# Kernel optimization log

Measured on AMD Instinct MI355X. Metric: run time of the kernel, lower is better.

The kernel has to match this reference:

```python
import jax, jax.numpy as jnp
import numpy as np

N = 100001      # item_num + 1
D = 64          # hidden_units
NNZ = 3200000   # number of nonzeros in encoder_adj (avg degree ~32)


def setup_inputs() -> dict:
    key = jax.random.key(0)
    k1, k2, k3, k4 = jax.random.split(key, 4)
    row_idx = jax.random.randint(k1, (NNZ,), 0, N, dtype=jnp.int32)
    col_idx = jax.random.randint(k2, (NNZ,), 0, N, dtype=jnp.int32)
    adj_vals = jax.random.uniform(k3, (NNZ,), dtype=jnp.float32)
    emb_weight = jax.random.normal(k4, (N, D), dtype=jnp.float32)
    return {"row_idx": row_idx, "col_idx": col_idx, "adj_vals": adj_vals,
            "emb_weight": emb_weight}


def _spmm(row_idx, col_idx, vals, x):
    # COO SpMM: out[r] += vals[e] * x[col[e]]  -> [N, D]
    gathered = vals[:, None] * x[col_idx]          # [NNZ, D]
    return jax.ops.segment_sum(gathered, row_idx, num_segments=N)


def reference(row_idx, col_idx, adj_vals, emb_weight):
    e0 = emb_weight                                 # ego embeddings
    e1 = _spmm(row_idx, col_idx, adj_vals, e0)      # GCN layer 1
    e2 = _spmm(row_idx, col_idx, adj_vals, e1)      # GCN layer 2
    summed = e0 + e1 + e2                           # sum(embeds)
    return (summed, e0, e1, e2)
```

## Files before the change

### kernel.cpp

```cpp
#include <hip/hip_runtime.h>
#include <stdint.h>

#define DHID 64
#define G_BLOCKS 256
#define BMAX 2048
#define RPB 64

static inline size_t align256(size_t x) { return (x + 255) & ~(size_t)255; }


__global__ void zero_f32(float* __restrict__ p, size_t n) {
  size_t i = (size_t)blockIdx.x * blockDim.x + threadIdx.x;
  if (i < n) p[i] = 0.f;
}


__global__ void a1_hist_k(const int* __restrict__ row, int* __restrict__ histGB,
                          int nnz, int B, int chunk) {
  __shared__ int h[BMAX];
  for (int i = threadIdx.x; i < B; i += blockDim.x) h[i] = 0;
  __syncthreads();
  int g = blockIdx.x;
  int s = g * chunk, e = min(nnz, s + chunk);
  for (int j = s + threadIdx.x; j < e; j += blockDim.x)
    atomicAdd(&h[row[j] >> 6], 1);
  __syncthreads();
  for (int i = threadIdx.x; i < B; i += blockDim.x)
    histGB[i * G_BLOCKS + g] = h[i];
}

__global__ void scan_gb_k(const int* __restrict__ histGB, int* __restrict__ offGB,
                          int* __restrict__ btot, int B) {
  __shared__ int wsum[4];
  int b = blockIdx.x, t = threadIdx.x, lane = t & 63, w = t >> 6;
  int v = histGB[b * G_BLOCKS + t];
  int incl = v;
#pragma unroll
  for (int off = 1; off < 64; off <<= 1) {
    int u = __shfl_up(incl, off);
    if (lane >= off) incl += u;
  }
  if (lane == 63) wsum[w] = incl;
  __syncthreads();
  int woff = 0;
  for (int w2 = 0; w2 < w; ++w2) woff += wsum[w2];
  offGB[b * G_BLOCKS + t] = woff + incl - v;
  if (t == 0) btot[b] = wsum[0] + wsum[1] + wsum[2] + wsum[3];
}

__global__ void scan_b_k(const int* __restrict__ btot, int* __restrict__ base, int B) {
  __shared__ int wsum[4];
  int t = threadIdx.x, lane = t & 63, w = t >> 6;
  int v[8];
  int s = 0;
#pragma unroll
  for (int i = 0; i < 8; ++i) {
    int idx = t * 8 + i;
    v[i] = (idx < B) ? btot[idx] : 0;
    s += v[i];
  }
  int incl = s;
#pragma unroll
  for (int off = 1; off < 64; off <<= 1) {
    int u = __shfl_up(incl, off);
    if (lane >= off) incl += u;
  }
  if (lane == 63) wsum[w] = incl;
  __syncthreads();
  int run = incl - s;
  for (int w2 = 0; w2 < w; ++w2) run += wsum[w2];
#pragma unroll
  for (int i = 0; i < 8; ++i) {
    int idx = t * 8 + i;
    if (idx <= B) base[idx] = run;
    run += v[i];
  }
}

__global__ void a2_scatter_k(const int* __restrict__ row, const int* __restrict__ col,
                             const float* __restrict__ val, const int* __restrict__ base,
                             const int* __restrict__ offGB, int2* __restrict__ stage,
                             int nnz, int B, int chunk) {
  __shared__ int cur[BMAX];
  int g = blockIdx.x;
  for (int i = threadIdx.x; i < B; i += blockDim.x)
    cur[i] = base[i] + offGB[i * G_BLOCKS + g];
  __syncthreads();
  int s = g * chunk, e = min(nnz, s + chunk);
  for (int j = s + threadIdx.x; j < e; j += blockDim.x) {
    int r = row[j];
    int b = r >> 6;
    int pos = atomicAdd(&cur[b], 1);
    int2 p;
    p.x = ((r & 63) << 24) | col[j];
    p.y = __float_as_int(val[j]);
    stage[pos] = p;
  }
}


__global__ __launch_bounds__(256) void
bgroup_k(const int* __restrict__ base, const int2* __restrict__ stage,
         int2* __restrict__ edges, int* __restrict__ rowstart, int n, int nnz) {
  __shared__ int h[RPB];
  __shared__ int cur[RPB];
  int b = blockIdx.x, t = threadIdx.x;
  if (t < RPB) h[t] = 0;
  __syncthreads();
  int s = base[b], e = base[b + 1];
  for (int j = s + t; j < e; j += 256)
    atomicAdd(&h[((unsigned)stage[j].x) >> 24], 1);
  __syncthreads();
  if (t < RPB) {
    int v = h[t];
    int incl = v;
#pragma unroll
    for (int off = 1; off < 64; off <<= 1) {
      int u = __shfl_up(incl, off);
      if (t >= off) incl += u;
    }
    int excl = incl - v;
    cur[t] = s + excl;
    int r = (b << 6) + t;
    if (r < n) rowstart[r] = s + excl;
  }
  if (b == 0 && t == 0) rowstart[n] = nnz;
  __syncthreads();
  for (int j = s + t; j < e; j += 256) {
    int2 p = stage[j];
    int rlow = ((unsigned)p.x) >> 24;
    int pos = atomicAdd(&cur[rlow], 1);
    int2 q;
    q.x = p.x & 0xFFFFFF;
    q.y = p.y;
    edges[pos] = q;
  }
}


__global__ void spmm_k(const int* __restrict__ rowstart, const int2* __restrict__ edges,
                       const float* __restrict__ x, float* __restrict__ y, int n) {
  int wave = (blockIdx.x * blockDim.x + threadIdx.x) >> 6;
  int lane = threadIdx.x & 63;
  if (wave >= n) return;
  int start = __builtin_amdgcn_readfirstlane(rowstart[wave]);
  int end   = __builtin_amdgcn_readfirstlane(rowstart[wave + 1]);
  float acc = 0.f;
  int k = start;
  for (; k + 8 <= end; k += 8) {
    int2 e0 = edges[k + 0], e1 = edges[k + 1], e2 = edges[k + 2], e3 = edges[k + 3];
    int2 e4 = edges[k + 4], e5 = edges[k + 5], e6 = edges[k + 6], e7 = edges[k + 7];
    float x0 = x[((size_t)e0.x << 6) + lane];
    float x1 = x[((size_t)e1.x << 6) + lane];
    float x2 = x[((size_t)e2.x << 6) + lane];
    float x3 = x[((size_t)e3.x << 6) + lane];
    float x4 = x[((size_t)e4.x << 6) + lane];
    float x5 = x[((size_t)e5.x << 6) + lane];
    float x6 = x[((size_t)e6.x << 6) + lane];
    float x7 = x[((size_t)e7.x << 6) + lane];
    acc += __int_as_float(e0.y) * x0;
    acc += __int_as_float(e1.y) * x1;
    acc += __int_as_float(e2.y) * x2;
    acc += __int_as_float(e3.y) * x3;
    acc += __int_as_float(e4.y) * x4;
    acc += __int_as_float(e5.y) * x5;
    acc += __int_as_float(e6.y) * x6;
    acc += __int_as_float(e7.y) * x7;
  }
  for (; k < end; ++k) {
    int2 e = edges[k];
    acc += __int_as_float(e.y) * x[((size_t)e.x << 6) + lane];
  }
  y[((size_t)wave << 6) + lane] = acc;
}

__global__ void spmm_fused_k(const int* __restrict__ rowstart, const int2* __restrict__ edges,
                             const float* __restrict__ e0, const float* __restrict__ e1,
                             float* __restrict__ e2, float* __restrict__ summed,
                             float* __restrict__ e0out, int n) {
  int wave = (blockIdx.x * blockDim.x + threadIdx.x) >> 6;
  int lane = threadIdx.x & 63;
  if (wave >= n) return;
  int start = __builtin_amdgcn_readfirstlane(rowstart[wave]);
  int end   = __builtin_amdgcn_readfirstlane(rowstart[wave + 1]);
  float acc = 0.f;
  int k = start;
  for (; k + 8 <= end; k += 8) {
    int2 ea = edges[k + 0], eb = edges[k + 1], ec = edges[k + 2], ed = edges[k + 3];
    int2 ee = edges[k + 4], ef = edges[k + 5], eg = edges[k + 6], eh = edges[k + 7];
    float x0 = e1[((size_t)ea.x << 6) + lane];
    float x1 = e1[((size_t)eb.x << 6) + lane];
    float x2 = e1[((size_t)ec.x << 6) + lane];
    float x3 = e1[((size_t)ed.x << 6) + lane];
    float x4 = e1[((size_t)ee.x << 6) + lane];
    float x5 = e1[((size_t)ef.x << 6) + lane];
    float x6 = e1[((size_t)eg.x << 6) + lane];
    float x7 = e1[((size_t)eh.x << 6) + lane];
    acc += __int_as_float(ea.y) * x0;
    acc += __int_as_float(eb.y) * x1;
    acc += __int_as_float(ec.y) * x2;
    acc += __int_as_float(ed.y) * x3;
    acc += __int_as_float(ee.y) * x4;
    acc += __int_as_float(ef.y) * x5;
    acc += __int_as_float(eg.y) * x6;
    acc += __int_as_float(eh.y) * x7;
  }
  for (; k < end; ++k) {
    int2 e = edges[k];
    acc += __int_as_float(e.y) * e1[((size_t)e.x << 6) + lane];
  }
  size_t o = ((size_t)wave << 6) + lane;
  float v0 = e0[o];
  float v1 = e1[o];
  e2[o] = acc;
  summed[o] = v0 + v1 + acc;
  e0out[o] = v0;
}


__global__ void spmm_atomic_k(const int* __restrict__ row, const int* __restrict__ col,
                              const float* __restrict__ val, const float* __restrict__ x,
                              float* __restrict__ y, int nnz) {
  int wave = (blockIdx.x * blockDim.x + threadIdx.x) >> 6;
  int lane = threadIdx.x & 63;
  if (wave >= nnz) return;
  int r = row[wave]; int c = col[wave]; float v = val[wave];
  atomicAdd(&y[(size_t)r * DHID + lane], v * x[(size_t)c * DHID + lane]);
}

__global__ void sum_k(const float4* __restrict__ e0, const float4* __restrict__ e1,
                      const float4* __restrict__ e2, float4* __restrict__ summed,
                      float4* __restrict__ e0out, int n4) {
  int i = blockIdx.x * blockDim.x + threadIdx.x;
  if (i < n4) {
    float4 a = e0[i], b = e1[i], c = e2[i];
    float4 s;
    s.x = a.x + b.x + c.x;
    s.y = a.y + b.y + c.y;
    s.z = a.z + b.z + c.z;
    s.w = a.w + b.w + c.w;
    summed[i] = s;
    e0out[i] = a;
  }
}

extern "C" void kernel_launch(void* const* d_in, const int* in_sizes, int n_in,
                              void* d_out, int out_size, void* d_ws, size_t ws_size,
                              hipStream_t stream) {
  const int*   row = (const int*)d_in[0];
  const int*   col = (const int*)d_in[1];
  const float* val = (const float*)d_in[2];
  const float* emb = (const float*)d_in[3];
  int nnz = in_sizes[0];
  int n   = in_sizes[3] / DHID;
  size_t ND = (size_t)n * DHID;

  float* out    = (float*)d_out;
  float* summed = out;
  float* e0o    = out + ND;
  float* e1     = out + 2 * ND;
  float* e2     = out + 3 * ND;

  int B  = (n + RPB - 1) / RPB;
  int chunk = (nnz + G_BLOCKS - 1) / G_BLOCKS;

  size_t o0 = 0;
  size_t histGB_off   = o0; o0 += align256((size_t)BMAX * G_BLOCKS * 4);
  size_t offGB_off    = o0; o0 += align256((size_t)BMAX * G_BLOCKS * 4);
  size_t btot_off     = o0; o0 += align256((size_t)BMAX * 4);
  size_t base_off     = o0; o0 += align256((size_t)(BMAX + 1) * 4);
  size_t rowstart_off = o0; o0 += align256((size_t)(n + 1) * 4);
  size_t stage_off    = o0; o0 += align256((size_t)nnz * 8);
  size_t edges_off    = o0; o0 += align256((size_t)nnz * 8);
  size_t need_sorted = o0;

  bool use_sorted = (ws_size >= need_sorted) && (B <= BMAX) && (n < (1 << 24));

  int rb = (int)((ND + 255) / 256);
  int n4 = (int)(ND / 4);
  int sb = (n4 + 255) / 256;
  int wb = (int)(((size_t)nnz * 64 + 255) / 256);

  if (use_sorted) {
    uint8_t* w = (uint8_t*)d_ws;
    int*  histGB   = (int*)(w + histGB_off);
    int*  offGB    = (int*)(w + offGB_off);
    int*  btot     = (int*)(w + btot_off);
    int*  base     = (int*)(w + base_off);
    int*  rowstart = (int*)(w + rowstart_off);
    int2* stage    = (int2*)(w + stage_off);
    int2* edges    = (int2*)(w + edges_off);

    a1_hist_k<<<G_BLOCKS, 256, 0, stream>>>(row, histGB, nnz, B, chunk);
    scan_gb_k<<<B, 256, 0, stream>>>(histGB, offGB, btot, B);
    scan_b_k<<<1, 256, 0, stream>>>(btot, base, B);
    a2_scatter_k<<<G_BLOCKS, 256, 0, stream>>>(row, col, val, base, offGB, stage,
                                               nnz, B, chunk);
    bgroup_k<<<B, 256, 0, stream>>>(base, stage, edges, rowstart, n, nnz);

    spmm_k<<<rb, 256, 0, stream>>>(rowstart, edges, emb, e1, n);
    spmm_fused_k<<<rb, 256, 0, stream>>>(rowstart, edges, emb, e1, e2, summed, e0o, n);
  } else {
    zero_f32<<<(int)((ND + 255) / 256), 256, 0, stream>>>(e1, ND);
    spmm_atomic_k<<<wb, 256, 0, stream>>>(row, col, val, emb, e1, nnz);
    zero_f32<<<(int)((ND + 255) / 256), 256, 0, stream>>>(e2, ND);
    spmm_atomic_k<<<wb, 256, 0, stream>>>(row, col, val, e1, e2, nnz);
    sum_k<<<sb, 256, 0, stream>>>((const float4*)emb, (const float4*)e1,
                                  (const float4*)e2, (float4*)summed,
                                  (float4*)e0o, n4);
  }
}
```

Measured before the change: 492.2 us.

## Widen CSR-build partitioning: more scatter blocks, 128-row buckets, unrolled atomic loops

Changes the two-pass COO-to-CSR bucket sort to use 1024 partition blocks and 128-row buckets (782 buckets) instead of 256 blocks and 64-row buckets. The scan kernel now handles four partition counts per thread, and the bucket-group kernel runs a two-wave scan over 128 rows. The histogram, scatter and group loops are unrolled by four so more independent loads are in flight before the LDS atomics. This targets the preprocessing cost of too few scatter blocks for the GPU. In exchange, the per-block histogram and offset tables are larger, and each bucket-group block now sorts twice as many edges.

```diff
diff --git a/kernel.cpp b/kernel.cpp
--- a/kernel.cpp
+++ b/kernel.cpp
@@ -2,9 +2,9 @@
 #include <stdint.h>
 
 #define DHID 64
-#define G_BLOCKS 256
-#define BMAX 2048
-#define RPB 64
+#define G_BLOCKS 1024
+#define BMAX 1024
+#define RPB 128
 
 static inline size_t align256(size_t x) { return (x + 255) & ~(size_t)255; }
 
@@ -15,26 +15,42 @@
 }
 
 
-__global__ void a1_hist_k(const int* __restrict__ row, int* __restrict__ histGB,
-                          int nnz, int B, int chunk) {
+__global__ __launch_bounds__(256) void
+a1_hist_k(const int* __restrict__ row, int* __restrict__ histGB,
+          int nnz, int B, int chunk) {
   __shared__ int h[BMAX];
-  for (int i = threadIdx.x; i < B; i += blockDim.x) h[i] = 0;
+  for (int i = threadIdx.x; i < B; i += 256) h[i] = 0;
   __syncthreads();
   int g = blockIdx.x;
   int s = g * chunk, e = min(nnz, s + chunk);
-  for (int j = s + threadIdx.x; j < e; j += blockDim.x)
-    atomicAdd(&h[row[j] >> 6], 1);
-  __syncthreads();
-  for (int i = threadIdx.x; i < B; i += blockDim.x)
+  int j = s + threadIdx.x;
+  for (; j + 768 < e; j += 1024) {
+    int r0 = row[j], r1 = row[j + 256], r2 = row[j + 512], r3 = row[j + 768];
+    atomicAdd(&h[r0 >> 7], 1);
+    atomicAdd(&h[r1 >> 7], 1);
+    atomicAdd(&h[r2 >> 7], 1);
+    atomicAdd(&h[r3 >> 7], 1);
+  }
+  for (; j < e; j += 256)
+    atomicAdd(&h[row[j] >> 7], 1);
+  __syncthreads();
+  for (int i = threadIdx.x; i < B; i += 256)
     histGB[i * G_BLOCKS + g] = h[i];
 }
 
-__global__ void scan_gb_k(const int* __restrict__ histGB, int* __restrict__ offGB,
-                          int* __restrict__ btot, int B) {
+__global__ __launch_bounds__(256) void
+scan_gb_k(const int* __restrict__ histGB, int* __restrict__ offGB,
+          int* __restrict__ btot, int B) {
   __shared__ int wsum[4];
   int b = blockIdx.x, t = threadIdx.x, lane = t & 63, w = t >> 6;
-  int v = histGB[b * G_BLOCKS + t];
-  int incl = v;
+  int v[4];
+  int s4 = 0;
+#pragma unroll
+  for (int i = 0; i < 4; ++i) {
+    v[i] = histGB[b * G_BLOCKS + t * 4 + i];
+    s4 += v[i];
+  }
+  int incl = s4;
 #pragma unroll
   for (int off = 1; off < 64; off <<= 1) {
     int u = __shfl_up(incl, off);
@@ -42,9 +58,13 @@
   }
   if (lane == 63) wsum[w] = incl;
   __syncthreads();
-  int woff = 0;
-  for (int w2 = 0; w2 < w; ++w2) woff += wsum[w2];
-  offGB[b * G_BLOCKS + t] = woff + incl - v;
+  int run = incl - s4;
+  for (int w2 = 0; w2 < w; ++w2) run += wsum[w2];
+#pragma unroll
+  for (int i = 0; i < 4; ++i) {
+    offGB[b * G_BLOCKS + t * 4 + i] = run;
+    run += v[i];
+  }
   if (t == 0) btot[b] = wsum[0] + wsum[1] + wsum[2] + wsum[3];
 }
 
@@ -77,22 +97,40 @@
   }
 }
 
-__global__ void a2_scatter_k(const int* __restrict__ row, const int* __restrict__ col,
-                             const float* __restrict__ val, const int* __restrict__ base,
-                             const int* __restrict__ offGB, int2* __restrict__ stage,
-                             int nnz, int B, int chunk) {
+__global__ __launch_bounds__(256) void
+a2_scatter_k(const int* __restrict__ row, const int* __restrict__ col,
+             const float* __restrict__ val, const int* __restrict__ base,
+             const int* __restrict__ offGB, int2* __restrict__ stage,
+             int nnz, int B, int chunk) {
   __shared__ int cur[BMAX];
   int g = blockIdx.x;
-  for (int i = threadIdx.x; i < B; i += blockDim.x)
+  for (int i = threadIdx.x; i < B; i += 256)
     cur[i] = base[i] + offGB[i * G_BLOCKS + g];
   __syncthreads();
   int s = g * chunk, e = min(nnz, s + chunk);
-  for (int j = s + threadIdx.x; j < e; j += blockDim.x) {
+  int j = s + threadIdx.x;
+  for (; j + 768 < e; j += 1024) {
+    int r0 = row[j], r1 = row[j + 256], r2 = row[j + 512], r3 = row[j + 768];
+    int c0 = col[j], c1 = col[j + 256], c2 = col[j + 512], c3 = col[j + 768];
+    float v0 = val[j], v1 = val[j + 256], v2 = val[j + 512], v3 = val[j + 768];
+    int p0 = atomicAdd(&cur[r0 >> 7], 1);
+    int p1 = atomicAdd(&cur[r1 >> 7], 1);
+    int p2 = atomicAdd(&cur[r2 >> 7], 1);
+    int p3 = atomicAdd(&cur[r3 >> 7], 1);
+    int2 q0; q0.x = ((r0 & 127) << 24) | c0; q0.y = __float_as_int(v0);
+    int2 q1; q1.x = ((r1 & 127) << 24) | c1; q1.y = __float_as_int(v1);
+    int2 q2; q2.x = ((r2 & 127) << 24) | c2; q2.y = __float_as_int(v2);
+    int2 q3; q3.x = ((r3 & 127) << 24) | c3; q3.y = __float_as_int(v3);
+    stage[p0] = q0;
+    stage[p1] = q1;
+    stage[p2] = q2;
+    stage[p3] = q3;
+  }
+  for (; j < e; j += 256) {
     int r = row[j];
-    int b = r >> 6;
-    int pos = atomicAdd(&cur[b], 1);
+    int pos = atomicAdd(&cur[r >> 7], 1);
     int2 p;
-    p.x = ((r & 63) << 24) | col[j];
+    p.x = ((r & 127) << 24) | col[j];
     p.y = __float_as_int(val[j]);
     stage[pos] = p;
   }
@@ -104,36 +142,73 @@
          int2* __restrict__ edges, int* __restrict__ rowstart, int n, int nnz) {
   __shared__ int h[RPB];
   __shared__ int cur[RPB];
+  __shared__ int w0sum;
   int b = blockIdx.x, t = threadIdx.x;
+  int lane = t & 63, w = t >> 6;
   if (t < RPB) h[t] = 0;
   __syncthreads();
   int s = base[b], e = base[b + 1];
-  for (int j = s + t; j < e; j += 256)
-    atomicAdd(&h[((unsigned)stage[j].x) >> 24], 1);
-  __syncthreads();
+  {
+    int j = s + t;
+    for (; j + 768 < e; j += 1024) {
+      int a0 = ((unsigned)stage[j].x) >> 24;
+      int a1 = ((unsigned)stage[j + 256].x) >> 24;
+      int a2 = ((unsigned)stage[j + 512].x) >> 24;
+      int a3 = ((unsigned)stage[j + 768].x) >> 24;
+      atomicAdd(&h[a0], 1);
+      atomicAdd(&h[a1], 1);
+      atomicAdd(&h[a2], 1);
+      atomicAdd(&h[a3], 1);
+    }
+    for (; j < e; j += 256)
+      atomicAdd(&h[((unsigned)stage[j].x) >> 24], 1);
+  }
+  __syncthreads();
+  int v = 0, incl = 0;
   if (t < RPB) {
-    int v = h[t];
-    int incl = v;
+    v = h[t];
+    incl = v;
 #pragma unroll
     for (int off = 1; off < 64; off <<= 1) {
       int u = __shfl_up(incl, off);
-      if (t >= off) incl += u;
+      if (lane >= off) incl += u;
     }
-    int excl = incl - v;
+    if (t == 63) w0sum = incl;
+  }
+  __syncthreads();
+  if (t < RPB) {
+    int excl = incl - v + ((w == 1) ? w0sum : 0);
     cur[t] = s + excl;
-    int r = (b << 6) + t;
+    int r = (b << 7) + t;
     if (r < n) rowstart[r] = s + excl;
   }
   if (b == 0 && t == 0) rowstart[n] = nnz;
   __syncthreads();
-  for (int j = s + t; j < e; j += 256) {
-    int2 p = stage[j];
-    int rlow = ((unsigned)p.x) >> 24;
-    int pos = atomicAdd(&cur[rlow], 1);
-    int2 q;
-    q.x = p.x & 0xFFFFFF;
-    q.y = p.y;
-    edges[pos] = q;
+  {
+    int j = s + t;
+    for (; j + 768 < e; j += 1024) {
+      int2 p0 = stage[j], p1 = stage[j + 256], p2 = stage[j + 512], p3 = stage[j + 768];
+      int q0 = atomicAdd(&cur[((unsigned)p0.x) >> 24], 1);
+      int q1 = atomicAdd(&cur[((unsigned)p1.x) >> 24], 1);
+      int q2 = atomicAdd(&cur[((unsigned)p2.x) >> 24], 1);
+      int q3 = atomicAdd(&cur[((unsigned)p3.x) >> 24], 1);
+      int2 o0; o0.x = p0.x & 0xFFFFFF; o0.y = p0.y;
+      int2 o1; o1.x = p1.x & 0xFFFFFF; o1.y = p1.y;
+      int2 o2; o2.x = p2.x & 0xFFFFFF; o2.y = p2.y;
+      int2 o3; o3.x = p3.x & 0xFFFFFF; o3.y = p3.y;
+      edges[q0] = o0;
+      edges[q1] = o1;
+      edges[q2] = o2;
+      edges[q3] = o3;
+    }
+    for (; j < e; j += 256) {
+      int2 p = stage[j];
+      int pos = atomicAdd(&cur[((unsigned)p.x) >> 24], 1);
+      int2 q;
+      q.x = p.x & 0xFFFFFF;
+      q.y = p.y;
+      edges[pos] = q;
+    }
   }
 }
 
@@ -265,10 +340,10 @@
   int chunk = (nnz + G_BLOCKS - 1) / G_BLOCKS;
 
   size_t o0 = 0;
-  size_t histGB_off   = o0; o0 += align256((size_t)BMAX * G_BLOCKS * 4);
-  size_t offGB_off    = o0; o0 += align256((size_t)BMAX * G_BLOCKS * 4);
-  size_t btot_off     = o0; o0 += align256((size_t)BMAX * 4);
-  size_t base_off     = o0; o0 += align256((size_t)(BMAX + 1) * 4);
+  size_t histGB_off   = o0; o0 += align256((size_t)B * G_BLOCKS * 4);
+  size_t offGB_off    = o0; o0 += align256((size_t)B * G_BLOCKS * 4);
+  size_t btot_off     = o0; o0 += align256((size_t)B * 4);
+  size_t base_off     = o0; o0 += align256((size_t)(B + 1) * 4);
   size_t rowstart_off = o0; o0 += align256((size_t)(n + 1) * 4);
   size_t stage_off    = o0; o0 += align256((size_t)nnz * 8);
   size_t edges_off    = o0; o0 += align256((size_t)nnz * 8);
```

New measurement: 433.1 us. 12.0% less time.
